# Optimization experiments

Hardware: AMD Instinct MI355X
Metric: run time of the kernel (lower is better)

Reference implementation:

```python
import jax, jax.numpy as jnp
import numpy as np

E = 1024  # embedding_dim
A = 1024  # attention_dim


def setup_inputs() -> dict:
    key = jax.random.key(0)
    k0, k1, k2, k3 = jax.random.split(key, 4)
    embedded = jax.random.normal(k0, (4, 4096, E), dtype=jnp.float32)
    # torch Linear weight is [out, in]; stored here as [in, out] for x @ W
    scale = 1.0 / np.sqrt(E)
    Wk = jax.random.uniform(k1, (E, A), dtype=jnp.float32, minval=-scale, maxval=scale)
    Wq = jax.random.uniform(k2, (E, A), dtype=jnp.float32, minval=-scale, maxval=scale)
    Wv = jax.random.uniform(k3, (E, A), dtype=jnp.float32, minval=-scale, maxval=scale)
    return {"embedded": embedded, "Wk": Wk, "Wq": Wq, "Wv": Wv}


def reference(embedded, Wk, Wq, Wv):
    B, T, C = embedded.shape
    K = embedded @ Wk  # [B,T,A]
    Q = embedded @ Wq
    V = embedded @ Wv
    d_k = Q.shape[-1]
    scores = jnp.einsum('bqa,bka->bqk', Q, K) / jnp.sqrt(jnp.float32(d_k))
    causal = jnp.tril(jnp.ones((T, T), dtype=bool))
    scores = jnp.where(causal, scores, -jnp.inf)
    attn = jax.nn.softmax(scores, axis=-1)
    out = jnp.einsum('bqk,bka->bqa', attn, V)
    return jnp.round(out, decimals=4)
```

## Files before the change

kernel.cpp:

```cpp
#include <hip/hip_runtime.h>
#include <hip/hip_fp16.h>

#define T_SEQ 4096
#define NBATCH 4
#define EDIM 1024
#define ADIM 1024
#define MTOT (NBATCH * T_SEQ)

typedef _Float16 f16x8 __attribute__((ext_vector_type(8)));
typedef float f32x4 __attribute__((ext_vector_type(4)));

#define STAGE(SRC, LD, LDSARR)                                               \
  {                                                                          \
    _Pragma("unroll") for (int t = 0; t < 2; ++t) {                          \
      const int rb = w * 2 + t;                                              \
      const _Float16* gsrc =                                                 \
          (SRC) + (size_t)(rb * 16 + (lane & 15)) * (LD) + (lane >> 4) * 8;  \
      __builtin_amdgcn_global_load_lds(                                      \
          (const __attribute__((address_space(1))) void*)gsrc,               \
          (__attribute__((address_space(3))) void*)&(LDSARR)[rb * 512], 16,  \
          0, 0);                                                             \
    }                                                                        \
  }

#define FRAG(LDSARR, B4, G) (*(const f16x8*)&(LDSARR)[((B4) * 4 + (G)) * 128 + lr * 8])

__global__ __launch_bounds__(256) void cast_x(const float* __restrict__ X,
                                              _Float16* __restrict__ Xh) {
  const size_t i = ((size_t)blockIdx.x * 256 + threadIdx.x) * 8;
  float4 a = ((const float4*)(X + i))[0];
  float4 b = ((const float4*)(X + i))[1];
  f16x8 o = {(_Float16)a.x, (_Float16)a.y, (_Float16)a.z, (_Float16)a.w,
             (_Float16)b.x, (_Float16)b.y, (_Float16)b.z, (_Float16)b.w};
  *(f16x8*)(Xh + i) = o;
}

__global__ __launch_bounds__(256) void cast_transpose_w(
    const float* __restrict__ Wk, const float* __restrict__ Wq,
    const float* __restrict__ Wv, _Float16* __restrict__ Wt) {
  __shared__ float tile[32][33];
  const int z = blockIdx.z;
  const float* W = (z == 0) ? Wk : (z == 1) ? Wq : Wv;
  const int n0 = blockIdx.x * 32, k0 = blockIdx.y * 32;
  const int tx = threadIdx.x, ty = threadIdx.y;
#pragma unroll
  for (int yy = 0; yy < 32; yy += 8)
    tile[ty + yy][tx] = W[(size_t)(k0 + ty + yy) * ADIM + n0 + tx];
  __syncthreads();
  _Float16* out = Wt + (size_t)z * EDIM * ADIM;
#pragma unroll
  for (int yy = 0; yy < 32; yy += 8)
    out[(size_t)(n0 + ty + yy) * EDIM + k0 + tx] = (_Float16)tile[tx][ty + yy];
}

__global__ __launch_bounds__(256) void gemm_qkv(
    const _Float16* __restrict__ Xh, const _Float16* __restrict__ Wt,
    _Float16* __restrict__ Qb, _Float16* __restrict__ Kb,
    _Float16* __restrict__ Vr) {
  const int z = blockIdx.z;
  const _Float16* Bt = Wt + (size_t)z * EDIM * ADIM;
  __shared__ __align__(16) _Float16 Al[8192];
  __shared__ __align__(16) _Float16 Bl[8192];
  const int tid = threadIdx.x;
  const int lane = tid & 63, w = tid >> 6;
  const int wm = w >> 1, wn = w & 1;
  const int lr = lane & 15, g = lane >> 4;
  const int h = blockIdx.y * gridDim.x + blockIdx.x;
  const int orig = (h & 7) * 128 + (h >> 3);
  const int m0 = (orig >> 3) * 128, n0 = (orig & 7) * 128;
  const _Float16* Abase = Xh + (size_t)m0 * EDIM;
  const _Float16* Bbase = Bt + (size_t)n0 * EDIM;

  f32x4 acc[4][4] = {};

  for (int k0 = 0; k0 < EDIM; k0 += 64) {
    STAGE(Abase + k0, EDIM, Al);
    STAGE(Abase + k0 + 32, EDIM, Al + 4096);
    STAGE(Bbase + k0, EDIM, Bl);
    STAGE(Bbase + k0 + 32, EDIM, Bl + 4096);
    __syncthreads();
#pragma unroll
    for (int s = 0; s < 2; ++s) {
      f16x8 af[4], bf[4];
#pragma unroll
      for (int i = 0; i < 4; i++) af[i] = FRAG(Al + s * 4096, wm * 4 + i, g);
#pragma unroll
      for (int j = 0; j < 4; j++) bf[j] = FRAG(Bl + s * 4096, wn * 4 + j, g);
#pragma unroll
      for (int i = 0; i < 4; i++)
#pragma unroll
        for (int j = 0; j < 4; j++)
          acc[i][j] = __builtin_amdgcn_mfma_f32_16x16x32_f16(af[i], bf[j], acc[i][j], 0, 0, 0);
    }
    __syncthreads();
  }

  _Float16* Outz = (z == 0) ? Kb : (z == 1) ? Qb : Vr;
#pragma unroll
  for (int i = 0; i < 4; i++)
#pragma unroll
    for (int j = 0; j < 4; j++)
#pragma unroll
      for (int r = 0; r < 4; r++) {
        const int row = m0 + wm * 64 + i * 16 + 4 * g + r;
        const int col = n0 + wn * 64 + j * 16 + lr;
        Outz[(size_t)row * ADIM + col] = (_Float16)acc[i][j][r];
      }
}

__global__ __launch_bounds__(256) void transpose_v(
    const _Float16* __restrict__ Vr, _Float16* __restrict__ Vt) {
  __shared__ _Float16 t[64][72];
  const int b = blockIdx.z;
  const int f0 = blockIdx.x * 64, t0 = blockIdx.y * 64;
  const int tid = threadIdx.x;
  const int c8 = tid & 7;
  const int r = tid >> 3;
  const _Float16* src = Vr + (size_t)b * T_SEQ * ADIM;
#pragma unroll
  for (int it = 0; it < 2; ++it) {
    const int tok = t0 + r + it * 32;
    *(f16x8*)&t[r + it * 32][c8 * 8] =
        *(const f16x8*)(src + (size_t)tok * ADIM + f0 + c8 * 8);
  }
  __syncthreads();
  _Float16* dst = Vt + (size_t)b * ADIM * T_SEQ;
#pragma unroll
  for (int it = 0; it < 2; ++it) {
    const int fr = r + it * 32;
    f16x8 o;
#pragma unroll
    for (int j = 0; j < 8; j++) o[j] = t[c8 * 8 + j][fr];
    *(f16x8*)(dst + (size_t)(f0 + fr) * T_SEQ + t0 + c8 * 8) = o;
  }
}

__global__ __launch_bounds__(256) void gemm_sqk(
    const _Float16* __restrict__ Qb, const _Float16* __restrict__ Kb,
    _Float16* __restrict__ Sb) {
  __shared__ __align__(16) _Float16 Al[8192];
  __shared__ __align__(16) _Float16 Bl[8192];
  const int b = blockIdx.y;
  const int tid = threadIdx.x;
  const int lane = tid & 63, w = tid >> 6;
  const int wm = w >> 1, wn = w & 1;
  const int lr = lane & 15, g = lane >> 4;
  const int h = blockIdx.x;
  const int orig = (h & 7) * 66 + (h >> 3);
  int bi = (int)((sqrtf(8.f * orig + 1.f) - 1.f) * 0.5f);
  while ((bi + 1) * (bi + 2) / 2 <= orig) ++bi;
  while (bi * (bi + 1) / 2 > orig) --bi;
  const int bj = orig - bi * (bi + 1) / 2;
  const int m0 = bi * 128, n0 = bj * 128;
  const _Float16* Abase = Qb + (size_t)b * T_SEQ * ADIM + (size_t)m0 * ADIM;
  const _Float16* Bbase = Kb + (size_t)b * T_SEQ * ADIM + (size_t)n0 * ADIM;

  f32x4 acc[4][4] = {};

  for (int k0 = 0; k0 < ADIM; k0 += 64) {
    STAGE(Abase + k0, ADIM, Al);
    STAGE(Abase + k0 + 32, ADIM, Al + 4096);
    STAGE(Bbase + k0, ADIM, Bl);
    STAGE(Bbase + k0 + 32, ADIM, Bl + 4096);
    __syncthreads();
#pragma unroll
    for (int s = 0; s < 2; ++s) {
      f16x8 af[4], bf[4];
#pragma unroll
      for (int i = 0; i < 4; i++) af[i] = FRAG(Al + s * 4096, wm * 4 + i, g);
#pragma unroll
      for (int j = 0; j < 4; j++) bf[j] = FRAG(Bl + s * 4096, wn * 4 + j, g);
#pragma unroll
      for (int i = 0; i < 4; i++)
#pragma unroll
        for (int j = 0; j < 4; j++)
          acc[i][j] = __builtin_amdgcn_mfma_f32_16x16x32_f16(af[i], bf[j], acc[i][j], 0, 0, 0);
    }
    __syncthreads();
  }

  _Float16* Srow = Sb + (size_t)b * T_SEQ * T_SEQ;
#pragma unroll
  for (int i = 0; i < 4; i++)
#pragma unroll
    for (int j = 0; j < 4; j++)
#pragma unroll
      for (int r = 0; r < 4; r++) {
        const int row = m0 + wm * 64 + i * 16 + 4 * g + r;
        const int col = n0 + wn * 64 + j * 16 + lr;
        Srow[(size_t)row * T_SEQ + col] = (_Float16)acc[i][j][r];
      }
}

__global__ __launch_bounds__(512) void softmax_rows(_Float16* __restrict__ S) {
  const int i = blockIdx.x, b = blockIdx.y;
  const int padded = ((i >> 7) + 1) << 7;
  const int tid = threadIdx.x;
  const int lane = tid & 63, w = tid >> 6;
  const int j0 = tid * 8;
  const bool active = j0 < padded;
  _Float16* row = S + ((size_t)b * T_SEQ + i) * T_SEQ;
  const float sm_scale = 0.03125f;

  float v[8];
  float m = -1e30f;
  if (active) {
    f16x8 x = *(const f16x8*)(row + j0);
#pragma unroll
    for (int jj = 0; jj < 8; jj++) {
      const float sv = (j0 + jj <= i) ? (float)x[jj] * sm_scale : -1e30f;
      v[jj] = sv;
      m = fmaxf(m, sv);
    }
  } else {
#pragma unroll
    for (int jj = 0; jj < 8; jj++) v[jj] = -1e30f;
  }
#pragma unroll
  for (int off = 1; off < 64; off <<= 1) m = fmaxf(m, __shfl_xor(m, off));
  __shared__ float redm[8], reds[8];
  if (lane == 0) redm[w] = m;
  __syncthreads();
#pragma unroll
  for (int ww = 0; ww < 8; ww++) m = fmaxf(m, redm[ww]);

  float s = 0.f;
#pragma unroll
  for (int jj = 0; jj < 8; jj++) {
    v[jj] = __expf(v[jj] - m);
    s += v[jj];
  }
#pragma unroll
  for (int off = 1; off < 64; off <<= 1) s += __shfl_xor(s, off);
  if (lane == 0) reds[w] = s;
  __syncthreads();
  s = 0.f;
#pragma unroll
  for (int ww = 0; ww < 8; ww++) s += reds[ww];
  const float inv = 1.f / s;

  if (active) {
    f16x8 o;
#pragma unroll
    for (int jj = 0; jj < 8; jj++) o[jj] = (_Float16)(v[jj] * inv);
    *(f16x8*)(row + j0) = o;
  }
}

__global__ __launch_bounds__(256) void gemm_pv(
    const _Float16* __restrict__ Pb, const _Float16* __restrict__ Vt,
    float* __restrict__ Part, float* __restrict__ Out) {
  __shared__ __align__(16) _Float16 Al[8192];
  __shared__ __align__(16) _Float16 Bl[8192];
  const int b = blockIdx.y;
  const int tid = threadIdx.x;
  const int lane = tid & 63, w = tid >> 6;
  const int wm = w >> 1, wn = w & 1;
  const int lr = lane & 15, g = lane >> 4;
  const int h = blockIdx.x;
  const int orig = (h & 7) * 48 + (h >> 3);
  int by, c, bx;
  if (orig < 128) {
    by = orig >> 3; c = 0; bx = orig & 7;
  } else {
    const int idx = orig - 128;
    by = 16 + (idx >> 4); c = (idx >> 3) & 1; bx = idx & 7;
  }
  const int m0 = by * 128, n0 = bx * 128;
  const int kbeg = c * 2048;
  const int kmax = (by + 1) * 128;
  const int kend = (c == 0) ? (kmax < 2048 ? kmax : 2048) : kmax;
  const _Float16* Abase = Pb + (size_t)b * T_SEQ * T_SEQ + (size_t)m0 * T_SEQ;
  const _Float16* Bbase = Vt + (size_t)b * ADIM * T_SEQ + (size_t)n0 * T_SEQ;

  f32x4 acc[4][4] = {};

  for (int k0 = kbeg; k0 < kend; k0 += 64) {
    STAGE(Abase + k0, T_SEQ, Al);
    STAGE(Abase + k0 + 32, T_SEQ, Al + 4096);
    STAGE(Bbase + k0, T_SEQ, Bl);
    STAGE(Bbase + k0 + 32, T_SEQ, Bl + 4096);
    __syncthreads();
#pragma unroll
    for (int s = 0; s < 2; ++s) {
      f16x8 af[4], bf[4];
#pragma unroll
      for (int i = 0; i < 4; i++) af[i] = FRAG(Al + s * 4096, wm * 4 + i, g);
#pragma unroll
      for (int j = 0; j < 4; j++) bf[j] = FRAG(Bl + s * 4096, wn * 4 + j, g);
#pragma unroll
      for (int i = 0; i < 4; i++)
#pragma unroll
        for (int j = 0; j < 4; j++)
          acc[i][j] = __builtin_amdgcn_mfma_f32_16x16x32_f16(af[i], bf[j], acc[i][j], 0, 0, 0);
    }
    __syncthreads();
  }

#pragma unroll
  for (int i = 0; i < 4; i++)
#pragma unroll
    for (int j = 0; j < 4; j++)
#pragma unroll
      for (int r = 0; r < 4; r++) {
        const int row = m0 + wm * 64 + i * 16 + 4 * g + r;
        const int col = n0 + wn * 64 + j * 16 + lr;
        if (c == 0)
          Out[((size_t)b * T_SEQ + row) * ADIM + col] = acc[i][j][r];
        else
          Part[((size_t)b * 2048 + (row - 2048)) * ADIM + col] = acc[i][j][r];
      }
}

__global__ __launch_bounds__(256) void reduce_pv(const float* __restrict__ Part,
                                                 float* __restrict__ Out) {
  const size_t id = (size_t)blockIdx.x * 256 + threadIdx.x;
  const int b = (int)(id >> 19);
  const size_t rem = id & 524287;
  const size_t row2 = rem >> 8, coli = rem & 255;
  float4* o = (float4*)Out + ((size_t)(b * 4096 + 2048) + row2) * 256 + coli;
  const float4* p = (const float4*)Part + ((size_t)b * 2048 + row2) * 256 + coli;
  float4 ov = *o;
  const float4 pv = *p;
  ov.x += pv.x; ov.y += pv.y; ov.z += pv.z; ov.w += pv.w;
  *o = ov;
}

extern "C" void kernel_launch(void* const* d_in, const int* in_sizes, int n_in,
                              void* d_out, int out_size, void* d_ws, size_t ws_size,
                              hipStream_t stream) {
  const float* X = (const float*)d_in[0];
  const float* Wk = (const float*)d_in[1];
  const float* Wq = (const float*)d_in[2];
  const float* Wv = (const float*)d_in[3];
  float* Out = (float*)d_out;

  char* ws = (char*)d_ws;
  const size_t WT_BYTES = (size_t)3 * EDIM * ADIM * 2;
  const size_t MAT_BYTES = (size_t)MTOT * ADIM * 2;
  _Float16* Wt = (_Float16*)ws;
  _Float16* Kb = (_Float16*)(ws + WT_BYTES);
  _Float16* Qb = (_Float16*)(ws + WT_BYTES + MAT_BYTES);
  _Float16* Vt = (_Float16*)(ws + WT_BYTES + 2 * MAT_BYTES);
  _Float16* Xh = (_Float16*)(ws + WT_BYTES + 3 * MAT_BYTES);
  _Float16* Sb = (_Float16*)(ws + WT_BYTES + 3 * MAT_BYTES);
  _Float16* Vr = (_Float16*)(ws + WT_BYTES + 4 * MAT_BYTES);
  float* Part = (float*)Qb;

  cast_x<<<dim3(MTOT * EDIM / 2048), dim3(256), 0, stream>>>(X, Xh);
  cast_transpose_w<<<dim3(32, 32, 3), dim3(32, 8), 0, stream>>>(Wk, Wq, Wv, Wt);
  gemm_qkv<<<dim3(8, 128, 3), dim3(256), 0, stream>>>(Xh, Wt, Qb, Kb, Vr);
  transpose_v<<<dim3(ADIM / 64, T_SEQ / 64, NBATCH), dim3(256), 0, stream>>>(Vr, Vt);
  gemm_sqk<<<dim3(528, NBATCH), dim3(256), 0, stream>>>(Qb, Kb, Sb);
  softmax_rows<<<dim3(T_SEQ, NBATCH), dim3(512), 0, stream>>>(Sb);
  gemm_pv<<<dim3(384, NBATCH), dim3(256), 0, stream>>>(Sb, Vt, Part, Out);
  reduce_pv<<<dim3(NBATCH * 2048 * 1024 / 4 / 256), dim3(256), 0, stream>>>(Part, Out);
}
```

Measured before the change: 701.0 us.

## Double-buffer LDS staging in GEMM k-loops to overlap loads with MFMA

Replaces the load-all-then-compute k-loop in the three GEMM kernels with a two-stage ping-pong pipeline over 32-wide k slices. The next slice is prefetched into the alternate LDS buffer with global_load_lds while MFMAs run on the current one, and a partial vmcnt wait lets the next slice stay in flight. The goal is to hide global-memory latency behind compute. In exchange there are more barriers per unit of work, since each iteration now covers half as much k, and correctness relies on the hand-written waitcnt and barrier ordering.

Result: no change. 698.8 us (-0.3%).

```diff
diff --git a/kernel.cpp b/kernel.cpp
--- a/kernel.cpp
+++ b/kernel.cpp
@@ -10,10 +10,15 @@
 typedef _Float16 f16x8 __attribute__((ext_vector_type(8)));
 typedef float f32x4 __attribute__((ext_vector_type(4)));
 
+#define WAITV4 asm volatile("s_waitcnt vmcnt(4)" ::: "memory")
+#define WAITV0 asm volatile("s_waitcnt vmcnt(0)" ::: "memory")
+#define FENCE asm volatile("" ::: "memory")
+#define BAR __builtin_amdgcn_s_barrier
+
 #define STAGE(SRC, LD, LDSARR)                                               \
   {                                                                          \
-    _Pragma("unroll") for (int t = 0; t < 2; ++t) {                          \
-      const int rb = w * 2 + t;                                              \
+    _Pragma("unroll") for (int t_ = 0; t_ < 2; ++t_) {                       \
+      const int rb = w * 2 + t_;                                             \
       const _Float16* gsrc =                                                 \
           (SRC) + (size_t)(rb * 16 + (lane & 15)) * (LD) + (lane >> 4) * 8;  \
       __builtin_amdgcn_global_load_lds(                                      \
@@ -24,6 +29,39 @@
   }
 
 #define FRAG(LDSARR, B4, G) (*(const f16x8*)&(LDSARR)[((B4) * 4 + (G)) * 128 + lr * 8])
+
+#define KLOOP(ABASE, BBASE, LD, KBEG, KEND)                                  \
+  {                                                                          \
+    STAGE((ABASE) + (KBEG), LD, Al);                                         \
+    STAGE((BBASE) + (KBEG), LD, Bl);                                         \
+    int cur = 0;                                                             \
+    const int NT = ((KEND) - (KBEG)) >> 5;                                   \
+    for (int t = 0; t < NT; ++t) {                                           \
+      const int nxt = cur ^ 1;                                               \
+      if (t + 1 < NT) {                                                      \
+        const int koff = (KBEG) + ((t + 1) << 5);                            \
+        STAGE((ABASE) + koff, LD, Al + nxt * 4096);                          \
+        STAGE((BBASE) + koff, LD, Bl + nxt * 4096);                          \
+        WAITV4;                                                              \
+      } else {                                                               \
+        WAITV0;                                                              \
+      }                                                                      \
+      BAR();                                                                 \
+      FENCE;                                                                 \
+      f16x8 af[4], bf[4];                                                    \
+      _Pragma("unroll") for (int i = 0; i < 4; i++)                          \
+          af[i] = FRAG(Al + cur * 4096, wm * 4 + i, g);                      \
+      _Pragma("unroll") for (int j = 0; j < 4; j++)                          \
+          bf[j] = FRAG(Bl + cur * 4096, wn * 4 + j, g);                      \
+      _Pragma("unroll") for (int i = 0; i < 4; i++)                          \
+          _Pragma("unroll") for (int j = 0; j < 4; j++)                      \
+              acc[i][j] = __builtin_amdgcn_mfma_f32_16x16x32_f16(            \
+                  af[i], bf[j], acc[i][j], 0, 0, 0);                         \
+      FENCE;                                                                 \
+      BAR();                                                                 \
+      cur = nxt;                                                             \
+    }                                                                        \
+  }
 
 __global__ __launch_bounds__(256) void cast_x(const float* __restrict__ X,
                                               _Float16* __restrict__ Xh) {
@@ -72,28 +110,7 @@
   const _Float16* Bbase = Bt + (size_t)n0 * EDIM;
 
   f32x4 acc[4][4] = {};
-
-  for (int k0 = 0; k0 < EDIM; k0 += 64) {
-    STAGE(Abase + k0, EDIM, Al);
-    STAGE(Abase + k0 + 32, EDIM, Al + 4096);
-    STAGE(Bbase + k0, EDIM, Bl);
-    STAGE(Bbase + k0 + 32, EDIM, Bl + 4096);
-    __syncthreads();
-#pragma unroll
-    for (int s = 0; s < 2; ++s) {
-      f16x8 af[4], bf[4];
-#pragma unroll
-      for (int i = 0; i < 4; i++) af[i] = FRAG(Al + s * 4096, wm * 4 + i, g);
-#pragma unroll
-      for (int j = 0; j < 4; j++) bf[j] = FRAG(Bl + s * 4096, wn * 4 + j, g);
-#pragma unroll
-      for (int i = 0; i < 4; i++)
-#pragma unroll
-        for (int j = 0; j < 4; j++)
-          acc[i][j] = __builtin_amdgcn_mfma_f32_16x16x32_f16(af[i], bf[j], acc[i][j], 0, 0, 0);
-    }
-    __syncthreads();
-  }
+  KLOOP(Abase, Bbase, EDIM, 0, EDIM);
 
   _Float16* Outz = (z == 0) ? Kb : (z == 1) ? Qb : Vr;
 #pragma unroll
@@ -156,28 +173,7 @@
   const _Float16* Bbase = Kb + (size_t)b * T_SEQ * ADIM + (size_t)n0 * ADIM;
 
   f32x4 acc[4][4] = {};
-
-  for (int k0 = 0; k0 < ADIM; k0 += 64) {
-    STAGE(Abase + k0, ADIM, Al);
-    STAGE(Abase + k0 + 32, ADIM, Al + 4096);
-    STAGE(Bbase + k0, ADIM, Bl);
-    STAGE(Bbase + k0 + 32, ADIM, Bl + 4096);
-    __syncthreads();
-#pragma unroll
-    for (int s = 0; s < 2; ++s) {
-      f16x8 af[4], bf[4];
-#pragma unroll
-      for (int i = 0; i < 4; i++) af[i] = FRAG(Al + s * 4096, wm * 4 + i, g);
-#pragma unroll
-      for (int j = 0; j < 4; j++) bf[j] = FRAG(Bl + s * 4096, wn * 4 + j, g);
-#pragma unroll
-      for (int i = 0; i < 4; i++)
-#pragma unroll
-        for (int j = 0; j < 4; j++)
-          acc[i][j] = __builtin_amdgcn_mfma_f32_16x16x32_f16(af[i], bf[j], acc[i][j], 0, 0, 0);
-    }
-    __syncthreads();
-  }
+  KLOOP(Abase, Bbase, ADIM, 0, ADIM);
 
   _Float16* Srow = Sb + (size_t)b * T_SEQ * T_SEQ;
 #pragma unroll
@@ -274,28 +270,7 @@
   const _Float16* Bbase = Vt + (size_t)b * ADIM * T_SEQ + (size_t)n0 * T_SEQ;
 
   f32x4 acc[4][4] = {};
-
-  for (int k0 = kbeg; k0 < kend; k0 += 64) {
-    STAGE(Abase + k0, T_SEQ, Al);
-    STAGE(Abase + k0 + 32, T_SEQ, Al + 4096);
-    STAGE(Bbase + k0, T_SEQ, Bl);
-    STAGE(Bbase + k0 + 32, T_SEQ, Bl + 4096);
-    __syncthreads();
-#pragma unroll
-    for (int s = 0; s < 2; ++s) {
-      f16x8 af[4], bf[4];
-#pragma unroll
-      for (int i = 0; i < 4; i++) af[i] = FRAG(Al + s * 4096, wm * 4 + i, g);
-#pragma unroll
-      for (int j = 0; j < 4; j++) bf[j] = FRAG(Bl + s * 4096, wn * 4 + j, g);
-#pragma unroll
-      for (int i = 0; i < 4; i++)
-#pragma unroll
-        for (int j = 0; j < 4; j++)
-          acc[i][j] = __builtin_amdgcn_mfma_f32_16x16x32_f16(af[i], bf[j], acc[i][j], 0, 0, 0);
-    }
-    __syncthreads();
-  }
+  KLOOP(Abase, Bbase, T_SEQ, kbeg, kend);
 
 #pragma unroll
   for (int i = 0; i < 4; i++)
```
